# Kernel optimization log

Hardware: AMD Instinct MI355X
Metric: run time of the kernel (lower is better)

Reference implementation:

```python
import jax, jax.numpy as jnp
import numpy as np

B, L, TOPK, NUM_RBF, NUM_POS, MAX_REL, CH = 4, 1024, 30, 16, 16, 32, 128
EDGE_IN = NUM_POS + NUM_RBF * 25 + 18  # 434
NODE_IN = 22


def _normalize(x, axis=-1):
    n = jnp.linalg.norm(x, axis=axis, keepdims=True)
    return jnp.where(n > 0, x / jnp.where(n > 0, n, 1.0), 0.0)


def layer_norm(x, g, b, eps=1e-5):
    mu = jnp.mean(x, axis=-1, keepdims=True)
    var = jnp.var(x, axis=-1, keepdims=True)
    return (x - mu) / jnp.sqrt(var + eps) * g + b


def gather_nodes_d(nodes, idx):
    # nodes [B,M,C], idx [B,N,K] -> [B,N,K,C]
    Bn, N, K = idx.shape
    out = jnp.take_along_axis(nodes, idx.reshape(Bn, N * K, 1), axis=1)
    return out.reshape(Bn, N, K, nodes.shape[-1])


def gather_edges(edges, idx):
    # edges [B,N,N,C], idx [B,N,K] -> [B,N,K,C]
    return jnp.take_along_axis(edges, idx[..., None], axis=2)


def cal_dihedral(Xf, eps=1e-7):
    U = _normalize(Xf[:, 1:, :] - Xf[:, :-1, :])
    u_0, u_1, u_2 = U[:, :-2], U[:, 1:-1], U[:, 2:]
    n_0 = _normalize(jnp.cross(u_0, u_1))
    n_1 = _normalize(jnp.cross(u_1, u_2))
    cosD = jnp.clip(jnp.sum(n_0 * n_1, -1), -1 + eps, 1 - eps)
    v = _normalize(jnp.cross(n_0, n_1))
    return jnp.sign(jnp.sum(-v * u_1, -1)) * jnp.arccos(cosD)


def _dihedrals(X, eps=1e-7):
    Bn, N = X.shape[0], X.shape[1]
    Xf = X[:, :, :3, :].reshape(Bn, 3 * N, 3)
    D = jnp.pad(cal_dihedral(Xf), ((0, 0), (1, 2))).reshape(Bn, N, 3)
    dihedral_feats = jnp.concatenate([jnp.cos(D), jnp.sin(D)], -1)
    U = _normalize(Xf[:, 1:, :] - Xf[:, :-1, :])
    cosA = jnp.clip(jnp.sum(U[:, :-2] * U[:, 1:-1], -1), -1 + eps, 1 - eps)
    A = jnp.pad(jnp.arccos(cosA), ((0, 0), (1, 2))).reshape(Bn, N, 3)
    angle_feats = jnp.concatenate([jnp.cos(A), jnp.sin(A)], -1)
    return jnp.concatenate([dihedral_feats, angle_feats], -1)  # [B,N,12]


def _quaternions(R):
    diag = jnp.diagonal(R, axis1=-2, axis2=-1)
    Rxx, Ryy, Rzz = diag[..., 0], diag[..., 1], diag[..., 2]
    mags = 0.5 * jnp.sqrt(jnp.abs(1.0 + jnp.stack([Rxx - Ryy - Rzz, -Rxx + Ryy - Rzz, -Rxx - Ryy + Rzz], -1)))
    signs = jnp.sign(jnp.stack([R[..., 2, 1] - R[..., 1, 2], R[..., 0, 2] - R[..., 2, 0], R[..., 1, 0] - R[..., 0, 1]], -1))
    w = jnp.sqrt(jax.nn.relu(1.0 + jnp.sum(diag, -1, keepdims=True))) / 2.0
    return _normalize(jnp.concatenate([signs * mags, w], -1))


def _orientations_coarse_gl_tuple(X, E_idx):
    V = X  # [B,N,4,3]
    Bn, N = X.shape[0], X.shape[1]
    Xf = X[:, :, :3, :].reshape(Bn, 3 * N, 3)
    U = _normalize(Xf[:, 1:, :] - Xf[:, :-1, :])
    u_0, u_1 = U[:, :-2], U[:, 1:-1]
    n_0 = _normalize(jnp.cross(u_0, u_1))[:, ::3]  # [B,N-1,3]
    b_1 = _normalize(u_0 - u_1)[:, ::3]
    Xa = Xf[:, ::3]  # N-atom coords [B,N,3]
    Q = jnp.stack([b_1, n_0, jnp.cross(b_1, n_0)], 2).reshape(Bn, N - 1, 9)
    Q = jnp.pad(Q, ((0, 0), (0, 1), (0, 0)))  # [B,N,9]
    Qm = Q.reshape(Bn, N, 3, 3)
    Q_neighbors = gather_nodes_d(Q, E_idx).reshape(Bn, N, -1, 3, 3)
    X_nb = gather_nodes_d(V[:, :, 1, :], E_idx)
    N_nb = gather_nodes_d(V[:, :, 0, :], E_idx)
    C_nb = gather_nodes_d(V[:, :, 2, :], E_idx)
    O_nb = gather_nodes_d(V[:, :, 3, :], E_idx)
    dXn = jnp.stack([X_nb, N_nb, C_nb, O_nb], 3) - Xa[:, :, None, None, :]  # [B,N,K,4,3]
    dU = jnp.einsum('bnij,bnkaj->bnkai', Qm, dXn)
    Kn = E_idx.shape[-1]
    E_direct = _normalize(dU).reshape(Bn, N, Kn, 12)
    R = jnp.einsum('bnji,bnkjl->bnkil', Qm, Q_neighbors)
    q = _quaternions(R)  # [B,N,K,4]
    dX_inner = V[:, :, jnp.array([0, 2, 3]), :] - Xa[:, :, None, :]
    V_direct = _normalize(jnp.einsum('bnij,bnaj->bnai', Qm, dX_inner)).reshape(Bn, N, 9)
    return V_direct, E_direct, q


def _dist(Xc, mask, eps=1e-6):
    mask_2D = mask[:, None, :] * mask[:, :, None]
    D = mask_2D * jnp.sqrt(jnp.sum((Xc[:, None, :, :] - Xc[:, :, None, :]) ** 2, -1) + eps)
    D_max = jnp.max(D, -1, keepdims=True)
    D_adjust = D + (1.0 - mask_2D) * D_max
    negD, E_idx = jax.lax.top_k(-D_adjust, min(TOPK, Xc.shape[1]))
    return -negD, E_idx


def _dist_seq(res_idx):
    D = jnp.abs(res_idx[:, :, None] - res_idx[:, None, :])
    _, E_idx = jax.lax.top_k(-D, min(TOPK, res_idx.shape[1]))
    return E_idx


def _rbf(D):
    D_mu = jnp.linspace(2.0, 22.0, NUM_RBF)
    D_sigma = (22.0 - 2.0) / NUM_RBF
    return jnp.exp(-(((D[..., None] - D_mu) / D_sigma) ** 2))


def _get_rbf(A, Bm, E_idx):
    D = jnp.sqrt(jnp.sum((A[:, :, None, :] - Bm[:, None, :, :]) ** 2, -1) + 1e-6)
    return _rbf(gather_edges(D[..., None], E_idx)[..., 0])


PAIRS = [('N', 'N'), ('C', 'C'), ('O', 'O'), ('Cb', 'Cb'), ('Ca', 'N'), ('Ca', 'C'), ('Ca', 'O'), ('Ca', 'Cb'),
         ('N', 'C'), ('N', 'O'), ('N', 'Cb'), ('Cb', 'C'), ('Cb', 'O'), ('O', 'C'), ('N', 'Ca'), ('C', 'Ca'),
         ('O', 'Ca'), ('Cb', 'Ca'), ('C', 'N'), ('O', 'N'), ('Cb', 'N'), ('C', 'Cb'), ('O', 'Cb'), ('C', 'O')]


def _forward(X, mask, residue_idx, chain_labels, W_pos, b_pos, W_edge, W_node, g_edge, b_edge, g_node, b_node):
    bvec = X[:, :, 1, :] - X[:, :, 0, :]
    cvec = X[:, :, 2, :] - X[:, :, 1, :]
    avec = jnp.cross(bvec, cvec)
    Cb = -0.58273431 * avec + 0.56802827 * bvec - 0.54067466 * cvec + X[:, :, 1, :]
    atoms = {'N': X[:, :, 0, :], 'Ca': X[:, :, 1, :], 'C': X[:, :, 2, :], 'O': X[:, :, 3, :], 'Cb': Cb}
    D_neighbors, E_idx = _dist(atoms['Ca'], mask)
    E_idx_res = _dist_seq(residue_idx)
    E_idx = jnp.where(mask[:, :, None] == 0, E_idx_res, E_idx)
    RBF_all = [_rbf(D_neighbors)]
    for pa, pb in PAIRS:
        RBF_all.append(_get_rbf(atoms[pa], atoms[pb], E_idx))
    RBF_all = jnp.concatenate(RBF_all, -1)  # [B,L,K,400]
    V_angles = _dihedrals(X) * mask[..., None]
    V_direct, E_direct, E_angles = _orientations_coarse_gl_tuple(X, E_idx)
    V_direct = V_direct * mask[..., None]
    offset = residue_idx[:, :, None] - residue_idx[:, None, :]
    E_offset = gather_edges(offset[..., None], E_idx)[..., 0]
    d_chains = (chain_labels[:, :, None] == chain_labels[:, None, :]).astype(jnp.int32)
    E_chains = gather_edges(d_chains[..., None], E_idx)[..., 0]
    d = jnp.clip(E_offset + MAX_REL, 0, 2 * MAX_REL) * E_chains + (1 - E_chains) * (2 * MAX_REL + 1)
    E_positional = jax.nn.one_hot(d, 2 * MAX_REL + 2, dtype=W_pos.dtype) @ W_pos + b_pos
    mask_j = gather_nodes_d(mask[..., None], E_idx)[..., 0]
    fdt = E_direct.dtype
    E = jnp.concatenate([E_positional, RBF_all, E_direct, E_angles,
                         E_chains[..., None].astype(fdt), mask_j[..., None]], -1)  # [B,L,K,434]
    E = layer_norm(E @ W_edge, g_edge, b_edge)
    Vn = jnp.concatenate([V_angles, V_direct, mask[..., None]], -1)  # [B,L,22]
    Vn = layer_norm(Vn @ W_node, g_node, b_node)
    return Vn, E, E_idx


def setup_inputs():
    key = jax.random.key(0)
    ks = jax.random.split(key, 8)
    X = 3.0 * jax.random.normal(ks[0], (B, L, 4, 3), jnp.float32)
    mask = jnp.ones((B, L), jnp.float32)
    residue_idx = jnp.tile(jnp.arange(L, dtype=jnp.int32), (B, 1))
    chain_labels = jax.random.randint(ks[1], (B, L), 0, 2, dtype=jnp.int32)
    s = lambda k, sh: jax.random.normal(k, sh, jnp.float32) * 0.05
    W_pos = s(ks[2], (2 * MAX_REL + 2, NUM_POS))
    b_pos = jnp.zeros((NUM_POS,), jnp.float32)
    W_edge = s(ks[3], (EDGE_IN, CH))
    W_node = s(ks[4], (NODE_IN, CH))
    return dict(X=X, mask=mask, residue_idx=residue_idx, chain_labels=chain_labels,
                W_pos=W_pos, b_pos=b_pos, W_edge=W_edge, W_node=W_node,
                g_edge=jnp.ones((CH,), jnp.float32), b_edge=jnp.zeros((CH,), jnp.float32),
                g_node=jnp.ones((CH,), jnp.float32), b_node=jnp.zeros((CH,), jnp.float32))


def reference(X, mask, residue_idx, chain_labels, W_pos, b_pos, W_edge, W_node, g_edge, b_edge, g_node, b_node):
    return _forward(X, mask, residue_idx, chain_labels, W_pos, b_pos, W_edge, W_node,
                    g_edge, b_edge, g_node, b_node)
```

## Files before the change

kernel.cpp:

```cpp
#include <hip/hip_runtime.h>

#define BATCH 4
#define LEN   1024
#define KNB   30
#define CH    128
#define EIN   434
#define KP    448
#define KST   14
#define ASTR  456
#define CSTR  132

typedef unsigned short ushort_t;
typedef __attribute__((ext_vector_type(8))) short bf16x8;
typedef __attribute__((ext_vector_type(4))) float f32x4;

__constant__ int c_pa[24] = {0,2,3,4,1,1,1,1,0,0,0,4,4,3,0,2,3,4,2,3,4,2,3,2};
__constant__ int c_pb[24] = {0,2,3,4,0,2,3,4,2,3,4,2,3,2,1,1,1,1,0,0,0,4,4,3};

struct F3 { float x, y, z; };
__device__ __forceinline__ F3 f3sub(F3 a, F3 b){ return {a.x-b.x, a.y-b.y, a.z-b.z}; }
__device__ __forceinline__ F3 f3cross(F3 a, F3 b){
  return {a.y*b.z - a.z*b.y, a.z*b.x - a.x*b.z, a.x*b.y - a.y*b.x};
}
__device__ __forceinline__ float f3dot(F3 a, F3 b){ return a.x*b.x + a.y*b.y + a.z*b.z; }
__device__ __forceinline__ F3 f3norm(F3 a){
  float s2 = f3dot(a,a);
  float inv = (s2 > 0.f) ? __builtin_amdgcn_rsqf(s2) : 0.f;
  return {a.x*inv, a.y*inv, a.z*inv};
}
__device__ __forceinline__ float fsign(float x){ return (x > 0.f) ? 1.f : ((x < 0.f) ? -1.f : 0.f); }
__device__ __forceinline__ float clip1(float c){ return fminf(fmaxf(c, -1.f + 1e-7f), 1.f - 1e-7f); }

__device__ __forceinline__ void dihedral_cs(F3 ua, F3 ub, F3 uc, float& c, float& s){
  F3 n0 = f3norm(f3cross(ua, ub));
  F3 n1 = f3norm(f3cross(ub, uc));
  float cd = clip1(f3dot(n0, n1));
  F3 v = f3norm(f3cross(n0, n1));
  c = cd;
  s = fsign(-f3dot(v, ub)) * sqrtf(1.f - cd*cd);
}

__device__ __forceinline__ ushort_t f2bf(float f){
  unsigned u = __float_as_uint(f);
  unsigned r = u + 0x7FFFu + ((u >> 16) & 1u);
  return (ushort_t)(r >> 16);
}

__device__ __forceinline__ unsigned cvt_pk(float a, float b){
  unsigned r;
  asm("v_cvt_pk_bf16_f32 %0, %1, %2" : "=v"(r) : "v"(a), "v"(b));
  return r;
}

#define DPP_MIN64_STEP(d, j, ctrl) do{                                        \
    unsigned td_ = (unsigned)__builtin_amdgcn_update_dpp(                     \
        (int)0xFFFFFFFF, (int)(d), (ctrl), 0xF, 0xF, false);                  \
    unsigned tj_ = (unsigned)__builtin_amdgcn_update_dpp(                     \
        (int)0xFFFFFFFF, (int)(j), (ctrl), 0xF, 0xF, false);                  \
    unsigned long long o_ = (((unsigned long long)td_) << 32) | tj_;          \
    unsigned long long c_ = (((unsigned long long)(d)) << 32) | (j);          \
    if (o_ < c_){ (d) = td_; (j) = tj_; }                                     \
  } while(0)
__device__ __forceinline__ void wave_min64(unsigned &d, unsigned &j){
  DPP_MIN64_STEP(d, j, 0x111);
  DPP_MIN64_STEP(d, j, 0x112);
  DPP_MIN64_STEP(d, j, 0x114);
  DPP_MIN64_STEP(d, j, 0x118);
  DPP_MIN64_STEP(d, j, 0x142);
  DPP_MIN64_STEP(d, j, 0x143);
  d = (unsigned)__builtin_amdgcn_readlane((int)d, 63);
  j = (unsigned)__builtin_amdgcn_readlane((int)j, 63);
}

__global__ __launch_bounds__(256) void prep_kernel(
    const float* __restrict__ X, const float* __restrict__ mask,
    const float* __restrict__ We,
    float* __restrict__ wCb, float* __restrict__ wQ, float* __restrict__ wVn,
    float* __restrict__ wCa, ushort_t* __restrict__ Wfrag)
{
  if (blockIdx.x >= 16){
    int f = (blockIdx.x - 16)*256 + threadIdx.x;
    if (f >= 8*KST*64) return;
    int t = f / (KST*64);
    int s = (f / 64) % KST;
    int l = f & 63;
    int n  = t*16 + (l & 15);
    int k0 = s*32 + (l >> 4)*8;
    ushort_t v[8];
    #pragma unroll
    for (int j = 0; j < 8; ++j){
      int k = k0 + j;
      v[j] = (k < EIN) ? f2bf(We[(size_t)k*CH + n]) : (ushort_t)0;
    }
    ulong2* dst = (ulong2*)(Wfrag + (size_t)f*8);
    *dst = *(ulong2*)v;
    return;
  }

  int idx = blockIdx.x * 256 + threadIdx.x;
  int n = idx & (LEN - 1);
  const float* p = X + (size_t)idx * 12;
  const float4* p4 = (const float4*)p;
  float4 q0 = p4[0], q1 = p4[1], q2 = p4[2];
  F3 Na = {q0.x, q0.y, q0.z};
  F3 Ca = {q0.w, q1.x, q1.y};
  F3 Cc = {q1.z, q1.w, q2.x};
  F3 Oa = {q2.y, q2.z, q2.w};
  ((float4*)wCa)[idx] = make_float4(Ca.x, Ca.y, Ca.z, 0.f);
  F3 bv = f3sub(Ca, Na);
  F3 cv = f3sub(Cc, Ca);
  F3 av = f3cross(bv, cv);
  wCb[idx*3+0] = -0.58273431f*av.x + 0.56802827f*bv.x - 0.54067466f*cv.x + Ca.x;
  wCb[idx*3+1] = -0.58273431f*av.y + 0.56802827f*bv.y - 0.54067466f*cv.y + Ca.y;
  wCb[idx*3+2] = -0.58273431f*av.z + 0.56802827f*bv.z - 0.54067466f*cv.z + Ca.z;

  F3 u0 = f3norm(bv);
  F3 u1 = f3norm(cv);

  float Q[9];
  if (n < LEN - 1){
    F3 b1 = f3norm(f3sub(u0, u1));
    F3 n0 = f3norm(f3cross(u0, u1));
    F3 r2 = f3cross(b1, n0);
    Q[0]=b1.x; Q[1]=b1.y; Q[2]=b1.z;
    Q[3]=n0.x; Q[4]=n0.y; Q[5]=n0.z;
    Q[6]=r2.x; Q[7]=r2.y; Q[8]=r2.z;
  } else {
    #pragma unroll
    for (int t = 0; t < 9; ++t) Q[t] = 0.f;
  }
  #pragma unroll
  for (int t = 0; t < 9; ++t) wQ[(size_t)idx*9 + t] = Q[t];

  float m = mask[idx];
  bool hp = (n > 0), hn = (n < LEN - 1);
  F3 um1 = {0,0,0}, u2 = {0,0,0}, u3 = {0,0,0};
  if (hp){
    const float* pp = p - 12;
    F3 Cp = {pp[6], pp[7], pp[8]};
    um1 = f3norm(f3sub(Na, Cp));
  }
  if (hn){
    const float* pn = p + 12;
    F3 Nn  = {pn[0], pn[1], pn[2]};
    F3 Can = {pn[3], pn[4], pn[5]};
    u2 = f3norm(f3sub(Nn, Cc));
    u3 = f3norm(f3sub(Can, Nn));
  }
  float cD0=1.f,sD0=0.f, cD1=1.f,sD1=0.f, cD2=1.f,sD2=0.f;
  float cA0=1.f,sA0=0.f, cA1=1.f,sA1=0.f, cA2=1.f,sA2=0.f;
  if (hp){
    dihedral_cs(um1, u0, u1, cD0, sD0);
    cA0 = clip1(f3dot(um1, u0)); sA0 = sqrtf(1.f - cA0*cA0);
  }
  if (hn){
    dihedral_cs(u0, u1, u2, cD1, sD1);
    dihedral_cs(u1, u2, u3, cD2, sD2);
    cA1 = clip1(f3dot(u0, u1)); sA1 = sqrtf(1.f - cA1*cA1);
    cA2 = clip1(f3dot(u1, u2)); sA2 = sqrtf(1.f - cA2*cA2);
  }
  float vn[22];
  vn[0] = cD0*m; vn[1] = cD1*m; vn[2]  = cD2*m;
  vn[3] = sD0*m; vn[4] = sD1*m; vn[5]  = sD2*m;
  vn[6] = cA0*m; vn[7] = cA1*m; vn[8]  = cA2*m;
  vn[9] = sA0*m; vn[10]= sA1*m; vn[11] = sA2*m;
  F3 dxs[3];
  dxs[0] = {0.f, 0.f, 0.f};
  dxs[1] = f3sub(Cc, Na);
  dxs[2] = f3sub(Oa, Na);
  #pragma unroll
  for (int a = 0; a < 3; ++a){
    F3 dv = dxs[a];
    F3 du = { Q[0]*dv.x + Q[1]*dv.y + Q[2]*dv.z,
              Q[3]*dv.x + Q[4]*dv.y + Q[5]*dv.z,
              Q[6]*dv.x + Q[7]*dv.y + Q[8]*dv.z };
    F3 dn = f3norm(du);
    vn[12 + a*3 + 0] = dn.x * m;
    vn[12 + a*3 + 1] = dn.y * m;
    vn[12 + a*3 + 2] = dn.z * m;
  }
  vn[21] = m;
  #pragma unroll
  for (int t = 0; t < 22; ++t) wVn[(size_t)idx*22 + t] = vn[t];
}

__global__ __launch_bounds__(256) void topk_kernel(
    const float* __restrict__ wCa, const float* __restrict__ wVn,
    const float* __restrict__ Wn,  const float* __restrict__ gn,
    const float* __restrict__ bn,
    float* __restrict__ wDn, int* __restrict__ wIdx,
    float* __restrict__ outI, float* __restrict__ outV)
{
  int wid = threadIdx.x >> 6, l = threadIdx.x & 63;
  int bi = blockIdx.x*4 + wid;
  int b  = bi >> 10;
  const float4* Ca = (const float4*)wCa;
  float4 ci = Ca[bi];
  const float4* Cb = Ca + (size_t)b * LEN;

  unsigned D[16];
  #pragma unroll
  for (int t = 0; t < 16; ++t){
    int j = l + 64*t;
    float4 cj = Cb[j];
    float dx = ci.x - cj.x, dy = ci.y - cj.y, dz = ci.z - cj.z;
    D[t] = __float_as_uint(sqrtf(dx*dx + dy*dy + dz*dz + 1e-6f));
  }
  unsigned lmin = D[0]; unsigned jmin = (unsigned)l;
  #pragma unroll
  for (int t = 1; t < 16; ++t)
    if (D[t] < lmin){ lmin = D[t]; jmin = (unsigned)(l + 64*t); }

  for (int k = 0; k < KNB; ++k){
    unsigned dmin = lmin, jw = jmin;
    wave_min64(dmin, jw);
    if (jmin == jw){
      wIdx[bi*KNB + k] = (int)jw;
      wDn[bi*KNB + k]  = __uint_as_float(dmin);
      outI[bi*KNB + k] = (float)jw;
      int tw = (int)(jw >> 6);
      #pragma unroll
      for (int t = 0; t < 16; ++t) if (t == tw) D[t] = 0xFFFFFFFFu;
      lmin = D[0]; jmin = (unsigned)l;
      #pragma unroll
      for (int t = 1; t < 16; ++t)
        if (D[t] < lmin){ lmin = D[t]; jmin = (unsigned)(l + 64*t); }
    }
  }

  float x0 = 0.f, x1 = 0.f;
  #pragma unroll
  for (int r = 0; r < 22; ++r){
    float vr = wVn[(size_t)bi*22 + r];
    x0 = fmaf(vr, Wn[r*CH + l],      x0);
    x1 = fmaf(vr, Wn[r*CH + l + 64], x1);
  }
  float sum = x0 + x1;
  #pragma unroll
  for (int off = 1; off < 64; off <<= 1) sum += __shfl_xor(sum, off);
  float mu = sum * (1.f/128.f);
  float d0 = x0 - mu, d1 = x1 - mu;
  float vs = d0*d0 + d1*d1;
  #pragma unroll
  for (int off = 1; off < 64; off <<= 1) vs += __shfl_xor(vs, off);
  float inv = 1.f / sqrtf(vs * (1.f/128.f) + 1e-5f);
  outV[(size_t)bi*CH + l]      = d0*inv*gn[l]    + bn[l];
  outV[(size_t)bi*CH + l + 64] = d1*inv*gn[l+64] + bn[l+64];
}

__device__ __forceinline__ void rbf_row(ushort_t* dst, float d){
  unsigned u[8];
  #pragma unroll
  for (int h = 0; h < 8; ++h){
    float t0 = d - (float)(2.0 + (2*h    ) * (20.0/15.0));
    float t1 = d - (float)(2.0 + (2*h + 1) * (20.0/15.0));
    float e0 = __builtin_amdgcn_exp2f(t0*t0 * -0.92332482f);
    float e1 = __builtin_amdgcn_exp2f(t1*t1 * -0.92332482f);
    u[h] = cvt_pk(e0, e1);
  }
  *(uint4*)&dst[0] = make_uint4(u[0], u[1], u[2], u[3]);
  *(uint4*)&dst[8] = make_uint4(u[4], u[5], u[6], u[7]);
}

__global__ __launch_bounds__(256) void edge_kernel(
    const float* __restrict__ X, const float* __restrict__ mask,
    const int* __restrict__ resi, const int* __restrict__ chain,
    const float* __restrict__ Wp, const float* __restrict__ bp,
    const float* __restrict__ ge, const float* __restrict__ be,
    const float* __restrict__ wCb, const float* __restrict__ wQ,
    const float* __restrict__ wDn, const int* __restrict__ wIdx,
    const ushort_t* __restrict__ Wfrag,
    float* __restrict__ outE)
{
  __shared__ __align__(16) ushort_t As[32*ASTR];
  __shared__ __align__(16) float sAJ[KNB][16];
  __shared__ float sAI[15];
  __shared__ float sQi[9];
  __shared__ float sQj[KNB][9];
  __shared__ int   sOffI[KNB];
  __shared__ float sChain[KNB];
  __shared__ float sMaskJ[KNB];
  __shared__ float sDn[KNB];

  int bi  = blockIdx.x;
  int b   = bi >> 10;
  int tid = threadIdx.x;

  if (tid < KNB){
    int j  = wIdx[bi*KNB + tid];
    int gj = (b << 10) + j;
    const float4* pj4 = (const float4*)(X + (size_t)gj * 12);
    float4 a0 = pj4[0], a1 = pj4[1], a2 = pj4[2];
    *(float4*)&sAJ[tid][0] = a0;
    *(float4*)&sAJ[tid][4] = a1;
    *(float4*)&sAJ[tid][8] = a2;
    sAJ[tid][12] = wCb[(size_t)gj*3 + 0];
    sAJ[tid][13] = wCb[(size_t)gj*3 + 1];
    sAJ[tid][14] = wCb[(size_t)gj*3 + 2];
    #pragma unroll
    for (int t = 0; t < 9; ++t) sQj[tid][t] = wQ[(size_t)gj*9 + t];
    sOffI[tid]  = resi[bi] - resi[gj];
    sChain[tid] = (chain[bi] == chain[gj]) ? 1.f : 0.f;
    sMaskJ[tid] = mask[gj];
    sDn[tid]    = wDn[bi*KNB + tid];
  } else if (tid == KNB){
    const float* pi = X + (size_t)bi * 12;
    #pragma unroll
    for (int t = 0; t < 12; ++t) sAI[t] = pi[t];
    sAI[12] = wCb[(size_t)bi*3 + 0];
    sAI[13] = wCb[(size_t)bi*3 + 1];
    sAI[14] = wCb[(size_t)bi*3 + 2];
  } else if (tid == KNB + 1){
    #pragma unroll
    for (int t = 0; t < 9; ++t) sQi[t] = wQ[(size_t)bi*9 + t];
  }
  for (int e = tid; e < KNB*14; e += 256){
    int r = e / 14, c = EIN + (e % 14);
    As[r*ASTR + c] = 0;
  }
  __syncthreads();

  if (tid < KNB*8){
    int k = tid >> 3, s = tid & 7;
    ushort_t* row = &As[k*ASTR];
    if (s == 0){
      int off = sOffI[k];
      float ch = sChain[k];
      int dpos = off + 32;
      dpos = dpos < 0 ? 0 : (dpos > 64 ? 64 : dpos);
      if (!(ch > 0.5f)) dpos = 65;
      const float4* wp4 = (const float4*)(Wp + dpos*16);
      const float4* bp4 = (const float4*)bp;
      unsigned u[8];
      #pragma unroll
      for (int h = 0; h < 4; ++h){
        float4 wv = wp4[h], bv = bp4[h];
        u[2*h]   = cvt_pk(wv.x + bv.x, wv.y + bv.y);
        u[2*h+1] = cvt_pk(wv.z + bv.z, wv.w + bv.w);
      }
      *(uint4*)&row[0] = make_uint4(u[0], u[1], u[2], u[3]);
      *(uint4*)&row[8] = make_uint4(u[4], u[5], u[6], u[7]);
      *(unsigned*)&row[432] = cvt_pk(ch, sMaskJ[k]);
    } else if (s == 1){
      float nx = sAI[0], ny = sAI[1], nz = sAI[2];
      const int amap[4] = {3, 0, 6, 9};
      float f[12];
      #pragma unroll
      for (int a = 0; a < 4; ++a){
        float dx = sAJ[k][amap[a]+0] - nx;
        float dy = sAJ[k][amap[a]+1] - ny;
        float dz = sAJ[k][amap[a]+2] - nz;
        float e0 = sQi[0]*dx + sQi[1]*dy + sQi[2]*dz;
        float e1 = sQi[3]*dx + sQi[4]*dy + sQi[5]*dz;
        float e2 = sQi[6]*dx + sQi[7]*dy + sQi[8]*dz;
        float ss = e0*e0 + e1*e1 + e2*e2;
        float inv = ss > 0.f ? __builtin_amdgcn_rsqf(ss) : 0.f;
        f[a*3+0] = e0*inv; f[a*3+1] = e1*inv; f[a*3+2] = e2*inv;
      }
      unsigned u[6];
      #pragma unroll
      for (int h = 0; h < 6; ++h) u[h] = cvt_pk(f[2*h], f[2*h+1]);
      *(uint4*)&row[416] = make_uint4(u[0], u[1], u[2], u[3]);
      *(uint2*)&row[424] = make_uint2(u[4], u[5]);
    } else if (s == 2){
      float R[3][3];
      #pragma unroll
      for (int i2 = 0; i2 < 3; ++i2)
        #pragma unroll
        for (int l2 = 0; l2 < 3; ++l2)
          R[i2][l2] = sQi[0*3+i2]*sQj[k][0*3+l2]
                    + sQi[1*3+i2]*sQj[k][1*3+l2]
                    + sQi[2*3+i2]*sQj[k][2*3+l2];
      float Rxx = R[0][0], Ryy = R[1][1], Rzz = R[2][2];
      float mx = 0.5f*sqrtf(fabsf(1.f + Rxx - Ryy - Rzz));
      float my = 0.5f*sqrtf(fabsf(1.f - Rxx + Ryy - Rzz));
      float mz = 0.5f*sqrtf(fabsf(1.f - Rxx - Ryy + Rzz));
      float qx = fsign(R[2][1] - R[1][2]) * mx;
      float qy = fsign(R[0][2] - R[2][0]) * my;
      float qz = fsign(R[1][0] - R[0][1]) * mz;
      float qw = sqrtf(fmaxf(1.f + Rxx + Ryy + Rzz, 0.f)) * 0.5f;
      float qn2 = qx*qx + qy*qy + qz*qz + qw*qw;
      float inv = qn2 > 0.f ? __builtin_amdgcn_rsqf(qn2) : 0.f;
      *(uint2*)&row[428] = make_uint2(cvt_pk(qx*inv, qy*inv), cvt_pk(qz*inv, qw*inv));
    }
    auto do_pair = [&](int p){
      float d;
      if (p == 0) d = sDn[k];
      else {
        int ai = c_pa[p-1]*3, bj = c_pb[p-1]*3;
        float dx = sAI[ai+0] - sAJ[k][bj+0];
        float dy = sAI[ai+1] - sAJ[k][bj+1];
        float dz = sAI[ai+2] - sAJ[k][bj+2];
        d = sqrtf(dx*dx + dy*dy + dz*dz + 1e-6f);
      }
      rbf_row(row + 16 + p*16, d);
    };
    for (int p = s; p < 24; p += 8) do_pair(p);
    if (s == 3) do_pair(24);
  }
  __syncthreads();

  int w = tid >> 6, l = tid & 63;
  int n0 = w*2;
  int aOff0 = (l & 15)*ASTR + (l >> 4)*8;
  int aOff1 = aOff0 + 16*ASTR;
  const ushort_t* bp0 = Wfrag + ((size_t)(n0    *KST)*64 + l)*8;
  const ushort_t* bp1 = Wfrag + ((size_t)((n0+1)*KST)*64 + l)*8;

  f32x4 acc00 = {0.f,0.f,0.f,0.f}, acc01 = acc00, acc10 = acc00, acc11 = acc00;

  bf16x8 a0 = *(const bf16x8*)&As[aOff0];
  bf16x8 a1 = *(const bf16x8*)&As[aOff1];
  bf16x8 b0 = *(const bf16x8*)bp0;
  bf16x8 b1 = *(const bf16x8*)bp1;
  #pragma unroll
  for (int s = 0; s < KST; ++s){
    bf16x8 a0n, a1n, b0n, b1n;
    if (s < KST-1){
      int ka = (s+1)*32;
      a0n = *(const bf16x8*)&As[aOff0 + ka];
      a1n = *(const bf16x8*)&As[aOff1 + ka];
      b0n = *(const bf16x8*)(bp0 + (size_t)(s+1)*64*8);
      b1n = *(const bf16x8*)(bp1 + (size_t)(s+1)*64*8);
    }
    acc00 = __builtin_amdgcn_mfma_f32_16x16x32_bf16(a0, b0, acc00, 0, 0, 0);
    acc01 = __builtin_amdgcn_mfma_f32_16x16x32_bf16(a0, b1, acc01, 0, 0, 0);
    acc10 = __builtin_amdgcn_mfma_f32_16x16x32_bf16(a1, b0, acc10, 0, 0, 0);
    acc11 = __builtin_amdgcn_mfma_f32_16x16x32_bf16(a1, b1, acc11, 0, 0, 0);
    if (s < KST-1){ a0 = a0n; a1 = a1n; b0 = b0n; b1 = b1n; }
  }
  __syncthreads();

  float* Cs = (float*)As;
  int ccol = l & 15, crow = (l >> 4)*4;
  #pragma unroll
  for (int r = 0; r < 4; ++r){
    Cs[(crow + r)*CSTR      + n0*16 + ccol]      = acc00[r];
    Cs[(crow + r)*CSTR      + (n0+1)*16 + ccol]  = acc01[r];
    Cs[(16 + crow + r)*CSTR + n0*16 + ccol]      = acc10[r];
    Cs[(16 + crow + r)*CSTR + (n0+1)*16 + ccol]  = acc11[r];
  }
  __syncthreads();

  if (tid < KNB*8){
    int row = tid >> 3, g = tid & 7;
    float v[16];
    #pragma unroll
    for (int c = 0; c < 16; ++c) v[c] = Cs[row*CSTR + g*16 + c];
    float s = 0.f;
    #pragma unroll
    for (int c = 0; c < 16; ++c) s += v[c];
    #pragma unroll
    for (int off = 1; off < 8; off <<= 1) s += __shfl_xor(s, off, 8);
    float mu = s * (1.f/128.f);
    float vs = 0.f;
    #pragma unroll
    for (int c = 0; c < 16; ++c){ float dd = v[c] - mu; vs += dd*dd; }
    #pragma unroll
    for (int off = 1; off < 8; off <<= 1) vs += __shfl_xor(vs, off, 8);
    float inv = 1.f / sqrtf(vs * (1.f/128.f) + 1e-5f);
    float o[16];
    #pragma unroll
    for (int c = 0; c < 16; ++c)
      o[c] = (v[c] - mu)*inv*ge[g*16 + c] + be[g*16 + c];
    float4* dst = (float4*)&outE[((size_t)bi*KNB + row)*CH + g*16];
    dst[0] = make_float4(o[0], o[1], o[2], o[3]);
    dst[1] = make_float4(o[4], o[5], o[6], o[7]);
    dst[2] = make_float4(o[8], o[9], o[10], o[11]);
    dst[3] = make_float4(o[12], o[13], o[14], o[15]);
  }
}

extern "C" void kernel_launch(void* const* d_in, const int* in_sizes, int n_in,
                              void* d_out, int out_size, void* d_ws, size_t ws_size,
                              hipStream_t stream)
{
  const float* X    = (const float*)d_in[0];
  const float* mask = (const float*)d_in[1];
  const int*   resi = (const int*)  d_in[2];
  const int*   chn  = (const int*)  d_in[3];
  const float* Wp   = (const float*)d_in[4];
  const float* bp   = (const float*)d_in[5];
  const float* We   = (const float*)d_in[6];
  const float* Wn   = (const float*)d_in[7];
  const float* ge   = (const float*)d_in[8];
  const float* be   = (const float*)d_in[9];
  const float* gn   = (const float*)d_in[10];
  const float* bn   = (const float*)d_in[11];

  float* outV = (float*)d_out;
  float* outE = outV + (size_t)BATCH*LEN*CH;
  float* outI = outE + (size_t)BATCH*LEN*KNB*CH;

  float* ws   = (float*)d_ws;
  float* wCb  = ws;
  float* wQ   = wCb + (size_t)BATCH*LEN*3;
  float* wVn  = wQ  + (size_t)BATCH*LEN*9;
  float* wDn  = wVn + (size_t)BATCH*LEN*22;
  int*   wIdx = (int*)(wDn + (size_t)BATCH*LEN*KNB);
  float* wCa  = (float*)(wIdx + (size_t)BATCH*LEN*KNB);
  ushort_t* Wfrag = (ushort_t*)(wCa + (size_t)BATCH*LEN*4);

  prep_kernel<<<16 + 28, 256, 0, stream>>>(X, mask, We, wCb, wQ, wVn, wCa, Wfrag);
  topk_kernel<<<BATCH*LEN/4, 256, 0, stream>>>(wCa, wVn, Wn, gn, bn,
                                               wDn, wIdx, outI, outV);
  edge_kernel<<<BATCH*LEN, 256, 0, stream>>>(X, mask, resi, chn, Wp, bp, ge, be,
                                             wCb, wQ, wDn, wIdx, Wfrag, outE);
}
```

Before: 180.2 us.

## Redistribute edge feature construction across all waves and vectorize workspace layouts

Edge-feature construction in the edge kernel is reorganized. Previously 240 threads each built one neighbor row across several stages. Now the 750 RBF tasks (30 neighbors by 25 atom pairs) are spread over all 256 threads, and the positional, orientation and quaternion features go to different waves. The per-neighbor gather is split across the four waves using float4 loads, after padding Cb and Q in the workspace to 4 and 12 floats. The RBF exponent is rewritten as a fused multiply-add in d. This aims to cut load imbalance and serial latency in the feature-building phase before the MFMA GEMM, at the cost of more complex indexing and a slightly larger workspace.

```diff
diff --git a/kernel.cpp b/kernel.cpp
--- a/kernel.cpp
+++ b/kernel.cpp
@@ -9,6 +9,7 @@
 #define KST   14
 #define ASTR  456
 #define CSTR  132
+#define AJS   20
 
 typedef unsigned short ushort_t;
 typedef __attribute__((ext_vector_type(8))) short bf16x8;
@@ -110,9 +111,10 @@
   F3 bv = f3sub(Ca, Na);
   F3 cv = f3sub(Cc, Ca);
   F3 av = f3cross(bv, cv);
-  wCb[idx*3+0] = -0.58273431f*av.x + 0.56802827f*bv.x - 0.54067466f*cv.x + Ca.x;
-  wCb[idx*3+1] = -0.58273431f*av.y + 0.56802827f*bv.y - 0.54067466f*cv.y + Ca.y;
-  wCb[idx*3+2] = -0.58273431f*av.z + 0.56802827f*bv.z - 0.54067466f*cv.z + Ca.z;
+  ((float4*)wCb)[idx] = make_float4(
+    -0.58273431f*av.x + 0.56802827f*bv.x - 0.54067466f*cv.x + Ca.x,
+    -0.58273431f*av.y + 0.56802827f*bv.y - 0.54067466f*cv.y + Ca.y,
+    -0.58273431f*av.z + 0.56802827f*bv.z - 0.54067466f*cv.z + Ca.z, 0.f);
 
   F3 u0 = f3norm(bv);
   F3 u1 = f3norm(cv);
@@ -129,8 +131,10 @@
     #pragma unroll
     for (int t = 0; t < 9; ++t) Q[t] = 0.f;
   }
-  #pragma unroll
-  for (int t = 0; t < 9; ++t) wQ[(size_t)idx*9 + t] = Q[t];
+  float4* wq4 = (float4*)(wQ + (size_t)idx*12);
+  wq4[0] = make_float4(Q[0], Q[1], Q[2], Q[3]);
+  wq4[1] = make_float4(Q[4], Q[5], Q[6], Q[7]);
+  wq4[2] = make_float4(Q[8], 0.f, 0.f, 0.f);
 
   float m = mask[idx];
   bool hp = (n > 0), hn = (n < LEN - 1);
@@ -248,20 +252,6 @@
   outV[(size_t)bi*CH + l + 64] = d1*inv*gn[l+64] + bn[l+64];
 }
 
-__device__ __forceinline__ void rbf_row(ushort_t* dst, float d){
-  unsigned u[8];
-  #pragma unroll
-  for (int h = 0; h < 8; ++h){
-    float t0 = d - (float)(2.0 + (2*h    ) * (20.0/15.0));
-    float t1 = d - (float)(2.0 + (2*h + 1) * (20.0/15.0));
-    float e0 = __builtin_amdgcn_exp2f(t0*t0 * -0.92332482f);
-    float e1 = __builtin_amdgcn_exp2f(t1*t1 * -0.92332482f);
-    u[h] = cvt_pk(e0, e1);
-  }
-  *(uint4*)&dst[0] = make_uint4(u[0], u[1], u[2], u[3]);
-  *(uint4*)&dst[8] = make_uint4(u[4], u[5], u[6], u[7]);
-}
-
 __global__ __launch_bounds__(256) void edge_kernel(
     const float* __restrict__ X, const float* __restrict__ mask,
     const int* __restrict__ resi, const int* __restrict__ chain,
@@ -273,46 +263,51 @@
     float* __restrict__ outE)
 {
   __shared__ __align__(16) ushort_t As[32*ASTR];
-  __shared__ __align__(16) float sAJ[KNB][16];
-  __shared__ float sAI[15];
-  __shared__ float sQi[9];
-  __shared__ float sQj[KNB][9];
-  __shared__ int   sOffI[KNB];
-  __shared__ float sChain[KNB];
-  __shared__ float sMaskJ[KNB];
-  __shared__ float sDn[KNB];
+  __shared__ __align__(16) float sAJ[KNB][AJS];
+  __shared__ __align__(16) float sAI[16];
+  __shared__ __align__(16) float sQi[12];
 
   int bi  = blockIdx.x;
   int b   = bi >> 10;
   int tid = threadIdx.x;
-
-  if (tid < KNB){
-    int j  = wIdx[bi*KNB + tid];
+  int w   = tid >> 6, l = tid & 63;
+
+  float qj0=0.f,qj1=0.f,qj2=0.f,qj3=0.f,qj4=0.f,qj5=0.f,qj6=0.f,qj7=0.f,qj8=0.f;
+  if (w == 0 && l < KNB){
+    int j  = wIdx[bi*KNB + l];
     int gj = (b << 10) + j;
     const float4* pj4 = (const float4*)(X + (size_t)gj * 12);
-    float4 a0 = pj4[0], a1 = pj4[1], a2 = pj4[2];
-    *(float4*)&sAJ[tid][0] = a0;
-    *(float4*)&sAJ[tid][4] = a1;
-    *(float4*)&sAJ[tid][8] = a2;
-    sAJ[tid][12] = wCb[(size_t)gj*3 + 0];
-    sAJ[tid][13] = wCb[(size_t)gj*3 + 1];
-    sAJ[tid][14] = wCb[(size_t)gj*3 + 2];
-    #pragma unroll
-    for (int t = 0; t < 9; ++t) sQj[tid][t] = wQ[(size_t)gj*9 + t];
-    sOffI[tid]  = resi[bi] - resi[gj];
-    sChain[tid] = (chain[bi] == chain[gj]) ? 1.f : 0.f;
-    sMaskJ[tid] = mask[gj];
-    sDn[tid]    = wDn[bi*KNB + tid];
-  } else if (tid == KNB){
-    const float* pi = X + (size_t)bi * 12;
-    #pragma unroll
-    for (int t = 0; t < 12; ++t) sAI[t] = pi[t];
-    sAI[12] = wCb[(size_t)bi*3 + 0];
-    sAI[13] = wCb[(size_t)bi*3 + 1];
-    sAI[14] = wCb[(size_t)bi*3 + 2];
-  } else if (tid == KNB + 1){
-    #pragma unroll
-    for (int t = 0; t < 9; ++t) sQi[t] = wQ[(size_t)bi*9 + t];
+    *(float4*)&sAJ[l][0] = pj4[0];
+    *(float4*)&sAJ[l][4] = pj4[1];
+    *(float4*)&sAJ[l][8] = pj4[2];
+  } else if (w == 1 && l < KNB){
+    int j  = wIdx[bi*KNB + l];
+    int gj = (b << 10) + j;
+    *(float4*)&sAJ[l][12] = ((const float4*)wCb)[gj];
+    sAJ[l][15] = wDn[bi*KNB + l];
+    sAJ[l][16] = (chain[bi] == chain[gj]) ? 1.f : 0.f;
+    sAJ[l][17] = mask[gj];
+    sAJ[l][18] = (float)(resi[bi] - resi[gj]);
+  } else if (w == 2 && l >= KNB && l < 2*KNB){
+    int k  = l - KNB;
+    int j  = wIdx[bi*KNB + k];
+    int gj = (b << 10) + j;
+    const float4* q4 = (const float4*)(wQ + (size_t)gj * 12);
+    float4 a = q4[0], bq = q4[1], cq = q4[2];
+    qj0=a.x; qj1=a.y; qj2=a.z; qj3=a.w;
+    qj4=bq.x; qj5=bq.y; qj6=bq.z; qj7=bq.w;
+    qj8=cq.x;
+  } else if (w == 3 && l == 0){
+    const float4* pi4 = (const float4*)(X + (size_t)bi * 12);
+    *(float4*)&sAI[0]  = pi4[0];
+    *(float4*)&sAI[4]  = pi4[1];
+    *(float4*)&sAI[8]  = pi4[2];
+    *(float4*)&sAI[12] = ((const float4*)wCb)[bi];
+  } else if (w == 3 && l == 1){
+    const float4* q4 = (const float4*)(wQ + (size_t)bi * 12);
+    *(float4*)&sQi[0] = q4[0];
+    *(float4*)&sQi[4] = q4[1];
+    *(float4*)&sQi[8] = q4[2];
   }
   for (int e = tid; e < KNB*14; e += 256){
     int r = e / 14, c = EIN + (e % 14);
@@ -320,12 +315,43 @@
   }
   __syncthreads();
 
-  if (tid < KNB*8){
-    int k = tid >> 3, s = tid & 7;
-    ushort_t* row = &As[k*ASTR];
-    if (s == 0){
-      int off = sOffI[k];
-      float ch = sChain[k];
+  auto rbf_task = [&](int tau){
+    int k = (int)(((unsigned)tau * 5243u) >> 17);
+    int p = tau - k*25;
+    float d;
+    if (p == 0) d = sAJ[k][15];
+    else {
+      int ai = c_pa[p-1]*3, bj = c_pb[p-1]*3;
+      float dx = sAI[ai+0] - sAJ[k][bj+0];
+      float dy = sAI[ai+1] - sAJ[k][bj+1];
+      float dz = sAI[ai+2] - sAJ[k][bj+2];
+      d = sqrtf(dx*dx + dy*dy + dz*dz + 1e-6f);
+    }
+    float A  = d*d*(-0.92332483f);
+    float Bc = d*1.84664966f;
+    ushort_t* dst = &As[k*ASTR + 16 + p*16];
+    unsigned u[8];
+    #pragma unroll
+    for (int h = 0; h < 8; ++h){
+      float mu0 = 2.f + (2*h  )*(4.f/3.f);
+      float mu1 = 2.f + (2*h+1)*(4.f/3.f);
+      float e0 = __builtin_amdgcn_exp2f(fmaf(Bc, mu0, A + (-0.92332483f*mu0*mu0)));
+      float e1 = __builtin_amdgcn_exp2f(fmaf(Bc, mu1, A + (-0.92332483f*mu1*mu1)));
+      u[h] = cvt_pk(e0, e1);
+    }
+    *(uint4*)&dst[0] = make_uint4(u[0], u[1], u[2], u[3]);
+    *(uint4*)&dst[8] = make_uint4(u[4], u[5], u[6], u[7]);
+  };
+
+  if (w == 0){
+    rbf_task(l); rbf_task(l+64); rbf_task(l+128); rbf_task(l+192);
+  } else if (w == 1){
+    rbf_task(256+l); rbf_task(320+l); rbf_task(384+l);
+    if (l < KNB){
+      int k = l;
+      ushort_t* row = &As[k*ASTR];
+      float ch = sAJ[k][16];
+      int off  = (int)sAJ[k][18];
       int dpos = off + 32;
       dpos = dpos < 0 ? 0 : (dpos > 64 ? 64 : dpos);
       if (!(ch > 0.5f)) dpos = 65;
@@ -340,8 +366,41 @@
       }
       *(uint4*)&row[0] = make_uint4(u[0], u[1], u[2], u[3]);
       *(uint4*)&row[8] = make_uint4(u[4], u[5], u[6], u[7]);
-      *(unsigned*)&row[432] = cvt_pk(ch, sMaskJ[k]);
-    } else if (s == 1){
+      *(unsigned*)&row[432] = cvt_pk(ch, sAJ[k][17]);
+    }
+  } else if (w == 2){
+    rbf_task(448+l); rbf_task(512+l);
+    if (l >= KNB && l < 2*KNB){
+      int k = l - KNB;
+      ushort_t* row = &As[k*ASTR];
+      float R[3][3];
+      R[0][0] = sQi[0]*qj0 + sQi[3]*qj3 + sQi[6]*qj6;
+      R[0][1] = sQi[0]*qj1 + sQi[3]*qj4 + sQi[6]*qj7;
+      R[0][2] = sQi[0]*qj2 + sQi[3]*qj5 + sQi[6]*qj8;
+      R[1][0] = sQi[1]*qj0 + sQi[4]*qj3 + sQi[7]*qj6;
+      R[1][1] = sQi[1]*qj1 + sQi[4]*qj4 + sQi[7]*qj7;
+      R[1][2] = sQi[1]*qj2 + sQi[4]*qj5 + sQi[7]*qj8;
+      R[2][0] = sQi[2]*qj0 + sQi[5]*qj3 + sQi[8]*qj6;
+      R[2][1] = sQi[2]*qj1 + sQi[5]*qj4 + sQi[8]*qj7;
+      R[2][2] = sQi[2]*qj2 + sQi[5]*qj5 + sQi[8]*qj8;
+      float Rxx = R[0][0], Ryy = R[1][1], Rzz = R[2][2];
+      float mx = 0.5f*sqrtf(fabsf(1.f + Rxx - Ryy - Rzz));
+      float my = 0.5f*sqrtf(fabsf(1.f - Rxx + Ryy - Rzz));
+      float mz = 0.5f*sqrtf(fabsf(1.f - Rxx - Ryy + Rzz));
+      float qx = fsign(R[2][1] - R[1][2]) * mx;
+      float qy = fsign(R[0][2] - R[2][0]) * my;
+      float qz = fsign(R[1][0] - R[0][1]) * mz;
+      float qw = sqrtf(fmaxf(1.f + Rxx + Ryy + Rzz, 0.f)) * 0.5f;
+      float qn2 = qx*qx + qy*qy + qz*qz + qw*qw;
+      float inv = qn2 > 0.f ? __builtin_amdgcn_rsqf(qn2) : 0.f;
+      *(uint2*)&row[428] = make_uint2(cvt_pk(qx*inv, qy*inv), cvt_pk(qz*inv, qw*inv));
+    }
+  } else {
+    rbf_task(576+l); rbf_task(640+l);
+    { int t2 = 704+l; if (t2 < 750) rbf_task(t2); }
+    if (l < KNB){
+      int k = l;
+      ushort_t* row = &As[k*ASTR];
       float nx = sAI[0], ny = sAI[1], nz = sAI[2];
       const int amap[4] = {3, 0, 6, 9};
       float f[12];
@@ -362,57 +421,22 @@
       for (int h = 0; h < 6; ++h) u[h] = cvt_pk(f[2*h], f[2*h+1]);
       *(uint4*)&row[416] = make_uint4(u[0], u[1], u[2], u[3]);
       *(uint2*)&row[424] = make_uint2(u[4], u[5]);
-    } else if (s == 2){
-      float R[3][3];
-      #pragma unroll
-      for (int i2 = 0; i2 < 3; ++i2)
-        #pragma unroll
-        for (int l2 = 0; l2 < 3; ++l2)
-          R[i2][l2] = sQi[0*3+i2]*sQj[k][0*3+l2]
-                    + sQi[1*3+i2]*sQj[k][1*3+l2]
-                    + sQi[2*3+i2]*sQj[k][2*3+l2];
-      float Rxx = R[0][0], Ryy = R[1][1], Rzz = R[2][2];
-      float mx = 0.5f*sqrtf(fabsf(1.f + Rxx - Ryy - Rzz));
-      float my = 0.5f*sqrtf(fabsf(1.f - Rxx + Ryy - Rzz));
-      float mz = 0.5f*sqrtf(fabsf(1.f - Rxx - Ryy + Rzz));
-      float qx = fsign(R[2][1] - R[1][2]) * mx;
-      float qy = fsign(R[0][2] - R[2][0]) * my;
-      float qz = fsign(R[1][0] - R[0][1]) * mz;
-      float qw = sqrtf(fmaxf(1.f + Rxx + Ryy + Rzz, 0.f)) * 0.5f;
-      float qn2 = qx*qx + qy*qy + qz*qz + qw*qw;
-      float inv = qn2 > 0.f ? __builtin_amdgcn_rsqf(qn2) : 0.f;
-      *(uint2*)&row[428] = make_uint2(cvt_pk(qx*inv, qy*inv), cvt_pk(qz*inv, qw*inv));
-    }
-    auto do_pair = [&](int p){
-      float d;
-      if (p == 0) d = sDn[k];
-      else {
-        int ai = c_pa[p-1]*3, bj = c_pb[p-1]*3;
-        float dx = sAI[ai+0] - sAJ[k][bj+0];
-        float dy = sAI[ai+1] - sAJ[k][bj+1];
-        float dz = sAI[ai+2] - sAJ[k][bj+2];
-        d = sqrtf(dx*dx + dy*dy + dz*dz + 1e-6f);
-      }
-      rbf_row(row + 16 + p*16, d);
-    };
-    for (int p = s; p < 24; p += 8) do_pair(p);
-    if (s == 3) do_pair(24);
+    }
   }
   __syncthreads();
 
-  int w = tid >> 6, l = tid & 63;
   int n0 = w*2;
   int aOff0 = (l & 15)*ASTR + (l >> 4)*8;
   int aOff1 = aOff0 + 16*ASTR;
-  const ushort_t* bp0 = Wfrag + ((size_t)(n0    *KST)*64 + l)*8;
-  const ushort_t* bp1 = Wfrag + ((size_t)((n0+1)*KST)*64 + l)*8;
+  const ushort_t* bpw0 = Wfrag + ((size_t)(n0    *KST)*64 + l)*8;
+  const ushort_t* bpw1 = Wfrag + ((size_t)((n0+1)*KST)*64 + l)*8;
 
   f32x4 acc00 = {0.f,0.f,0.f,0.f}, acc01 = acc00, acc10 = acc00, acc11 = acc00;
 
   bf16x8 a0 = *(const bf16x8*)&As[aOff0];
   bf16x8 a1 = *(const bf16x8*)&As[aOff1];
-  bf16x8 b0 = *(const bf16x8*)bp0;
-  bf16x8 b1 = *(const bf16x8*)bp1;
+  bf16x8 b0 = *(const bf16x8*)bpw0;
+  bf16x8 b1 = *(const bf16x8*)bpw1;
   #pragma unroll
   for (int s = 0; s < KST; ++s){
     bf16x8 a0n, a1n, b0n, b1n;
@@ -420,8 +444,8 @@
       int ka = (s+1)*32;
       a0n = *(const bf16x8*)&As[aOff0 + ka];
       a1n = *(const bf16x8*)&As[aOff1 + ka];
-      b0n = *(const bf16x8*)(bp0 + (size_t)(s+1)*64*8);
-      b1n = *(const bf16x8*)(bp1 + (size_t)(s+1)*64*8);
+      b0n = *(const bf16x8*)(bpw0 + (size_t)(s+1)*64*8);
+      b1n = *(const bf16x8*)(bpw1 + (size_t)(s+1)*64*8);
     }
     acc00 = __builtin_amdgcn_mfma_f32_16x16x32_bf16(a0, b0, acc00, 0, 0, 0);
     acc01 = __builtin_amdgcn_mfma_f32_16x16x32_bf16(a0, b1, acc01, 0, 0, 0);
@@ -444,9 +468,10 @@
 
   if (tid < KNB*8){
     int row = tid >> 3, g = tid & 7;
-    float v[16];
-    #pragma unroll
-    for (int c = 0; c < 16; ++c) v[c] = Cs[row*CSTR + g*16 + c];
+    const float4* vr = (const float4*)&Cs[row*CSTR + g*16];
+    float4 v0 = vr[0], v1 = vr[1], v2 = vr[2], v3 = vr[3];
+    float v[16] = {v0.x,v0.y,v0.z,v0.w, v1.x,v1.y,v1.z,v1.w,
+                   v2.x,v2.y,v2.z,v2.w, v3.x,v3.y,v3.z,v3.w};
     float s = 0.f;
     #pragma unroll
     for (int c = 0; c < 16; ++c) s += v[c];
@@ -494,8 +519,8 @@
 
   float* ws   = (float*)d_ws;
   float* wCb  = ws;
-  float* wQ   = wCb + (size_t)BATCH*LEN*3;
-  float* wVn  = wQ  + (size_t)BATCH*LEN*9;
+  float* wQ   = wCb + (size_t)BATCH*LEN*4;
+  float* wVn  = wQ  + (size_t)BATCH*LEN*12;
   float* wDn  = wVn + (size_t)BATCH*LEN*22;
   int*   wIdx = (int*)(wDn + (size_t)BATCH*LEN*KNB);
   float* wCa  = (float*)(wIdx + (size_t)BATCH*LEN*KNB);
```

After: 171.8 us. 4.6% less time.
